# Optimization experiments

Hardware: AMD Instinct MI355X
Metric: run time of the kernel (lower is better)

The kernel has to match this reference:

```python
import jax, jax.numpy as jnp
import numpy as np

B, CIN, COUT, H, W, LAT, G = 4, 128, 256, 64, 64, 256, 16
EPS = 1e-5


def _bn(x, p):
    # p: [4, C] stacked (gamma, beta, running_mean, running_var); eval-mode BN over channel dim 1
    g, b, m, v = p
    sh = (1, -1) + (1,) * (x.ndim - 2)
    return (x - m.reshape(sh)) * (g.reshape(sh) * jax.lax.rsqrt(v.reshape(sh) + EPS)) + b.reshape(sh)


def _prelu(x, a):
    return jnp.where(x > 0, x, a * x)


def _pool(x):
    b, c, h, w = x.shape
    return x.reshape(b, c, h // 2, 2, w // 2, 2).mean((3, 5))


def _conv1x1(w, x):
    return jnp.einsum('oc,bchw->bohw', w, x)


def _cbn(x, latent, bnp, lin):
    y = _bn(x, bnp)
    sb = latent @ lin.T  # [B, 2C]
    s, b = jnp.split(sb, 2, axis=-1)
    return y * s[:, :, None, None] + b[:, :, None, None]


def _axial(x, wqkv, bn_qkv, bn_sim, bn_out, rel, dim):
    # x: [B, C, H, W]; attend along H (dim==0) or W (dim==1)
    x = x.transpose(0, 3, 1, 2) if dim == 0 else x.transpose(0, 2, 1, 3)
    b, d1, c, s = x.shape
    x = x.reshape(b * d1, c, s)
    qkv = _bn(jnp.einsum('oc,bcs->bos', wqkv, x), bn_qkv)  # [bN, 2*COUT, S]
    gc = COUT // G
    qkv = qkv.reshape(b * d1, G, 2 * gc, s)
    q, k, v = qkv[:, :, :gc // 2], qkv[:, :, gc // 2:gc], qkv[:, :, gc:]
    idx = jnp.arange(s)[:, None] - jnp.arange(s)[None, :] + s - 1
    emb = rel[:, idx]  # [2*gc, S, S]
    qe, ke, ve = emb[:gc // 2], emb[gc // 2:gc], emb[gc:]
    q_emb = jnp.einsum('bgci,cij->bgij', q, qe)
    k_emb = jnp.einsum('bgci,cij->bgij', k, ke)
    # torch reinterprets [b,g,S,S] as 'bgci': contraction over the 3rd axis
    qk = jnp.einsum('bgki,bgkj->bgij', q_emb, k_emb)
    sim = jnp.concatenate([qk, q_emb, k_emb], axis=1)  # [bN, 3G, S, S]
    sim = _bn(sim, bn_sim)
    sim = sim.reshape(b * d1, 3, G, s, s).sum(1)
    sim = jax.nn.softmax(sim, axis=-1)
    att = jnp.einsum('bgij,bgcj->bgci', sim, v)
    att_e = jnp.einsum('bgij,cij->bgci', sim, ve)
    o = jnp.stack([att, att_e], axis=3).reshape(b * d1, 2 * COUT, s)
    o = _bn(o, bn_out)
    o = o.reshape(b, d1, COUT, 2, s).sum(3)
    return o.transpose(0, 2, 3, 1) if dim == 0 else o.transpose(0, 2, 1, 3)


def _bn_params(key, c):
    k1, k2, k3, k4 = jax.random.split(key, 4)
    return jnp.stack([1.0 + 0.1 * jax.random.normal(k1, (c,)),
                      0.1 * jax.random.normal(k2, (c,)),
                      0.05 * jax.random.normal(k3, (c,)),
                      jax.random.uniform(k4, (c,), minval=0.5, maxval=1.5)])


def setup_inputs() -> dict:
    key = jax.random.key(0)
    ks = list(jax.random.split(key, 24))
    gc = COUT // G
    inp = {
        'x': jax.random.normal(ks[0], (B, CIN, H, W), dtype=jnp.float32),
        'latent': jax.random.normal(ks[1], (B, LAT), dtype=jnp.float32),
        'w_in': 0.1 * jax.random.normal(ks[2], (COUT, CIN)),
        'bn_in': _bn_params(ks[3], COUT),
        'lin_in': 0.1 * jax.random.normal(ks[4], (2 * COUT, LAT)),
        'alpha_in': jnp.array(0.25, dtype=jnp.float32),
        'a0_wqkv': 0.1 * jax.random.normal(ks[5], (2 * COUT, COUT)),
        'a0_bn_qkv': _bn_params(ks[6], 2 * COUT),
        'a0_bn_sim': _bn_params(ks[7], 3 * G),
        'a0_bn_out': _bn_params(ks[8], 2 * COUT),
        'a0_rel': 0.1 * jax.random.normal(ks[9], (2 * gc, 2 * H - 1)),
        'a1_wqkv': 0.1 * jax.random.normal(ks[10], (2 * COUT, COUT)),
        'a1_bn_qkv': _bn_params(ks[11], 2 * COUT),
        'a1_bn_sim': _bn_params(ks[12], 3 * G),
        'a1_bn_out': _bn_params(ks[13], 2 * COUT),
        'a1_rel': 0.1 * jax.random.normal(ks[14], (2 * gc, 2 * W - 1)),
        'w_out': 0.1 * jax.random.normal(ks[15], (COUT, COUT)),
        'bn_out': _bn_params(ks[16], COUT),
        'lin_out': 0.1 * jax.random.normal(ks[17], (2 * COUT, LAT)),
        'w_res': 0.1 * jax.random.normal(ks[18], (COUT, CIN)),
        'alpha_fin': jnp.array(0.25, dtype=jnp.float32),
    }
    return inp


def reference(x, latent, w_in, bn_in, lin_in, alpha_in,
              a0_wqkv, a0_bn_qkv, a0_bn_sim, a0_bn_out, a0_rel,
              a1_wqkv, a1_bn_qkv, a1_bn_sim, a1_bn_out, a1_rel,
              w_out, bn_out, lin_out, w_res, alpha_fin):
    out = _prelu(_cbn(_conv1x1(w_in, x), latent, bn_in, lin_in), alpha_in)
    out = _axial(out, a0_wqkv, a0_bn_qkv, a0_bn_sim, a0_bn_out, a0_rel, 0)
    out = _axial(out, a1_wqkv, a1_bn_qkv, a1_bn_sim, a1_bn_out, a1_rel, 1)
    out = _cbn(_conv1x1(w_out, _pool(out)), latent, bn_out, lin_out)
    out = out + _pool(_conv1x1(w_res, x))
    return _prelu(out, alpha_fin)
```

## Files before the change

### kernel.cpp

```cpp
#include <hip/hip_runtime.h>
#include <hip/hip_bf16.h>

#define EPS_F 1e-5f

typedef __attribute__((ext_vector_type(8))) _Float16 f16x8;
typedef __attribute__((ext_vector_type(4))) _Float16 f16x4;
typedef __attribute__((ext_vector_type(4))) float f32x4;

union U16x8 { ushort u[8]; _Float16 h[8]; f16x8 v; };

static __device__ inline ushort f2h(float f) {
  _Float16 h = (_Float16)f;
  return __builtin_bit_cast(ushort, h);
}
static __device__ inline float h2f(ushort u) {
  return (float)__builtin_bit_cast(_Float16, u);
}

__global__ void __launch_bounds__(256) prep_kernel(
    const float* __restrict__ w_in, const float* __restrict__ a0w,
    const float* __restrict__ a1w, const float* __restrict__ w_out,
    const float* __restrict__ w_res,
    const float* __restrict__ latent, const float* __restrict__ lin_in,
    const float* __restrict__ lin_out,
    const float* __restrict__ a0_rel, const float* __restrict__ a1_rel,
    const float* __restrict__ x,
    ushort* __restrict__ w16, ushort* __restrict__ relimg,
    float* __restrict__ sb_in, float* __restrict__ sb_out,
    ushort* __restrict__ x16, ushort* __restrict__ pool_x) {
  const int gid = blockIdx.x;
  const int tid = threadIdx.x;
  __shared__ __align__(16) char lsm[10240];

  if (gid < 1608) {
    int idx = gid * 256 + tid;
    if (idx < 393216) {
      const float* src; int off;
      if (idx < 32768)       { src = w_in;  off = 0; }
      else if (idx < 163840) { src = a0w;   off = 32768; }
      else if (idx < 294912) { src = a1w;   off = 163840; }
      else if (idx < 360448) { src = w_out; off = 294912; }
      else                   { src = w_res; off = 360448; }
      w16[idx] = f2h(src[idx - off]);
    } else if (idx < 397312) {
      int r = idx - 393216;
      int which = r >> 11;
      int rr = r & 2047;
      int b = rr >> 9, k = rr & 511;
      const float* lin = which ? lin_out : lin_in;
      const float* lv = latent + b * 256;
      const float* lr = lin + k * 256;
      float acc = 0.f;
#pragma unroll 8
      for (int l = 0; l < 256; ++l) acc += lv[l] * lr[l];
      (which ? sb_out : sb_in)[b * 512 + k] = acc;
    } else if (idx < 411648) {
      int e = idx - 397312;
      int which = e >= 7168;
      int s = which ? e - 7168 : e;
      const float* rel = which ? a1_rel : a0_rel;
      ushort val = 0;
      if (s < 2560) {
        int d = s / 20, c = s % 20;
        if (c < 8 && d < 127) val = f2h(rel[c * 127 + d]);
      } else if (s < 5120) {
        int s2 = s - 2560;
        int d = s2 / 20, c = s2 % 20;
        if (c >= 8 && c < 16 && d < 127) val = f2h(rel[c * 127 + d]);
      } else {
        int pos = (s - 5120) * 2;
        int c = pos >> 8;
        int inner = (pos & 255) ^ ((c & 7) << 4);
        int d = inner >> 1;
        if (d < 127) val = f2h(rel[(16 + c) * 127 + d]);
      }
      relimg[which * 7168 + s] = val;
    }
  } else if (gid < 2120) {
    int e = gid - 1608;
    int pt = e & 31, ct = (e >> 5) & 3, b = e >> 7;
    ushort (*Lt)[40] = (ushort(*)[40])lsm;
#pragma unroll
    for (int r = 0; r < 16; ++r) {
      int e2 = tid + 256 * r;
      int c = e2 >> 7, p = e2 & 127;
      Lt[p][c] = f2h(x[((size_t)(b * 128 + ct * 32 + c)) * 4096 + pt * 128 + p]);
    }
    __syncthreads();
#pragma unroll
    for (int r = 0; r < 2; ++r) {
      int e2 = tid + 256 * r;
      int p = e2 >> 2, q = e2 & 3;
      *(f16x8*)&x16[((size_t)b * 4096 + pt * 128 + p) * 128 + ct * 32 + 8 * q] =
          *(const f16x8*)&Lt[p][8 * q];
    }
  } else {
    int e = gid - 2120;
    int ip = e & 31, ct = (e >> 5) & 3, b = e >> 7;
    float (*Lp)[33] = (float(*)[33])lsm;
    {
      int c = tid >> 3, grp = tid & 7;
      const float* base = x + ((size_t)(b * 128 + ct * 32 + c)) * 4096 + (2 * ip) * 64 + 8 * grp;
      float4 a0 = *(const float4*)&base[0];
      float4 a1 = *(const float4*)&base[4];
      float4 b0 = *(const float4*)&base[64];
      float4 b1 = *(const float4*)&base[68];
      Lp[c][4 * grp + 0] = 0.25f * (a0.x + a0.y + b0.x + b0.y);
      Lp[c][4 * grp + 1] = 0.25f * (a0.z + a0.w + b0.z + b0.w);
      Lp[c][4 * grp + 2] = 0.25f * (a1.x + a1.y + b1.x + b1.y);
      Lp[c][4 * grp + 3] = 0.25f * (a1.z + a1.w + b1.z + b1.w);
    }
    __syncthreads();
    {
      int jp = tid >> 3, q = tid & 7;
      ushort4 o;
      o.x = f2h(Lp[4 * q + 0][jp]);
      o.y = f2h(Lp[4 * q + 1][jp]);
      o.z = f2h(Lp[4 * q + 2][jp]);
      o.w = f2h(Lp[4 * q + 3][jp]);
      *(ushort4*)&pool_x[((size_t)b * 1024 + ip * 32 + jp) * 128 + ct * 32 + 4 * q] = o;
    }
  }
}

template <int MODE>
__global__ void __launch_bounds__(256) conv_mfma_kernel(
    const ushort* __restrict__ X, const ushort* __restrict__ W16,
    ushort* __restrict__ Y16, int Cin, int Cout, int P,
    const float* __restrict__ bn, const float* __restrict__ sb,
    const float* __restrict__ alpha) {
  const int tid = threadIdx.x;
  const int p0 = blockIdx.x * 128;
  const int o0 = blockIdx.y * 64;
  const int b  = blockIdx.z;
  const int lane = tid & 63;
  const int wv = tid >> 6;
  const int m = lane & 15, h = lane >> 4;
  const int wr = wv >> 1, wc = wv & 1;

  __shared__ __align__(16) char smem[27648];
  ushort (*Xs)[72] = (ushort(*)[72])smem;
  ushort (*Ws)[72] = (ushort(*)[72])(smem + 18432);
  ushort (*Es)[72] = (ushort(*)[72])smem;

  f32x4 acc[2][4];
#pragma unroll
  for (int i = 0; i < 2; ++i)
#pragma unroll
    for (int j = 0; j < 4; ++j) acc[i][j] = (f32x4){0.f, 0.f, 0.f, 0.f};

  const ushort* Xb = X + (size_t)b * P * Cin;

  for (int k0 = 0; k0 < Cin; k0 += 64) {
    __syncthreads();
#pragma unroll
    for (int r = 0; r < 4; ++r) {
      int e = tid + 256 * r;
      int pp = e >> 3, ch = e & 7;
      *(f16x8*)&Xs[pp][8 * ch] =
          *(const f16x8*)&Xb[(size_t)(p0 + pp) * Cin + k0 + 8 * ch];
    }
#pragma unroll
    for (int r = 0; r < 2; ++r) {
      int e = tid + 256 * r;
      int oc = e >> 3, ch = e & 7;
      *(f16x8*)&Ws[oc][8 * ch] =
          *(const f16x8*)&W16[(size_t)(o0 + oc) * Cin + k0 + 8 * ch];
    }
    __syncthreads();
#pragma unroll
    for (int ks = 0; ks < 2; ++ks) {
      f16x8 af[2], bf[4];
#pragma unroll
      for (int t = 0; t < 2; ++t) af[t] = *(const f16x8*)&Ws[32 * wr + 16 * t + m][32 * ks + 8 * h];
#pragma unroll
      for (int t = 0; t < 4; ++t) bf[t] = *(const f16x8*)&Xs[64 * wc + 16 * t + m][32 * ks + 8 * h];
#pragma unroll
      for (int ta = 0; ta < 2; ++ta)
#pragma unroll
        for (int tb = 0; tb < 4; ++tb)
          acc[ta][tb] = __builtin_amdgcn_mfma_f32_16x16x32_f16(af[ta], bf[tb], acc[ta][tb], 0, 0, 0);
    }
  }

  float scl[2][4], shf[2][4];
#pragma unroll
  for (int ta = 0; ta < 2; ++ta)
#pragma unroll
    for (int r = 0; r < 4; ++r) {
      int oc = o0 + 32 * wr + 16 * ta + 4 * h + r;
      float scale = 1.f, shift = 0.f;
      if (MODE & 1) {
        float sc = bn[oc] * rsqrtf(bn[3 * Cout + oc] + EPS_F);
        scale = sc;
        shift = bn[Cout + oc] - bn[2 * Cout + oc] * sc;
      }
      if (MODE & 2) {
        float ss = sb[b * 2 * Cout + oc];
        float bb = sb[b * 2 * Cout + Cout + oc];
        scale *= ss;
        shift = shift * ss + bb;
      }
      scl[ta][r] = scale; shf[ta][r] = shift;
    }
  float al = (MODE & 8) ? *alpha : 0.f;

  __syncthreads();
#pragma unroll
  for (int ta = 0; ta < 2; ++ta)
#pragma unroll
    for (int tb = 0; tb < 4; ++tb)
#pragma unroll
      for (int r = 0; r < 4; ++r) {
        float v = acc[ta][tb][r] * scl[ta][r] + shf[ta][r];
        if (MODE & 8) v = v > 0.f ? v : al * v;
        Es[64 * wc + 16 * tb + m][32 * wr + 16 * ta + 4 * h + r] = f2h(v);
      }
  __syncthreads();
#pragma unroll
  for (int r = 0; r < 4; ++r) {
    int e = tid + 256 * r;
    int pp = e >> 3, q = e & 7;
    *(f16x8*)&Y16[((size_t)b * P + p0 + pp) * Cout + o0 + 8 * q] =
        *(const f16x8*)&Es[pp][8 * q];
  }
}

__global__ void __launch_bounds__(256) final_fused_kernel(
    const ushort* __restrict__ t0, const ushort* __restrict__ pool_x,
    const ushort* __restrict__ Wo, const ushort* __restrict__ Wr,
    float* __restrict__ Y32,
    const float* __restrict__ bn, const float* __restrict__ sb,
    const float* __restrict__ alpha) {
  const int tid = threadIdx.x;
  const int p0 = blockIdx.x * 128;
  const int o0 = blockIdx.y * 64;
  const int b  = blockIdx.z;
  const int lane = tid & 63;
  const int wv = tid >> 6;
  const int m = lane & 15, h = lane >> 4;
  const int wr = wv >> 1, wc = wv & 1;

  __shared__ __align__(16) char smem[27648];
  ushort (*Xs)[72] = (ushort(*)[72])smem;
  ushort (*Ws)[72] = (ushort(*)[72])(smem + 18432);

  f32x4 acc1[2][4], acc2[2][4];
#pragma unroll
  for (int i = 0; i < 2; ++i)
#pragma unroll
    for (int j = 0; j < 4; ++j) {
      acc1[i][j] = (f32x4){0.f, 0.f, 0.f, 0.f};
      acc2[i][j] = (f32x4){0.f, 0.f, 0.f, 0.f};
    }

  for (int k0 = 0; k0 < 256; k0 += 64) {
    __syncthreads();
#pragma unroll
    for (int r = 0; r < 4; ++r) {
      int e = tid + 256 * r;
      int pp = e >> 3, ch = e & 7;
      int pg = p0 + pp;
      int ip = pg >> 5, jp = pg & 31;
      size_t tb = ((size_t)b * 4096 + ip * 128 + jp * 2) * 256 + k0 + 8 * ch;
      U16x8 a, bb, c, d, o;
      a.v  = *(const f16x8*)&t0[tb];
      bb.v = *(const f16x8*)&t0[tb + 256];
      c.v  = *(const f16x8*)&t0[tb + 64 * 256];
      d.v  = *(const f16x8*)&t0[tb + 65 * 256];
#pragma unroll
      for (int e2 = 0; e2 < 8; ++e2)
        o.h[e2] = ((a.h[e2] + bb.h[e2]) + (c.h[e2] + d.h[e2])) * (_Float16)0.25f;
      *(f16x8*)&Xs[pp][8 * ch] = o.v;
    }
#pragma unroll
    for (int r = 0; r < 2; ++r) {
      int e = tid + 256 * r;
      int oc = e >> 3, ch = e & 7;
      *(f16x8*)&Ws[oc][8 * ch] = *(const f16x8*)&Wo[(size_t)(o0 + oc) * 256 + k0 + 8 * ch];
    }
    __syncthreads();
#pragma unroll
    for (int ks = 0; ks < 2; ++ks) {
      f16x8 af[2], bf[4];
#pragma unroll
      for (int t = 0; t < 2; ++t) af[t] = *(const f16x8*)&Ws[32 * wr + 16 * t + m][32 * ks + 8 * h];
#pragma unroll
      for (int t = 0; t < 4; ++t) bf[t] = *(const f16x8*)&Xs[64 * wc + 16 * t + m][32 * ks + 8 * h];
#pragma unroll
      for (int ta = 0; ta < 2; ++ta)
#pragma unroll
        for (int tb2 = 0; tb2 < 4; ++tb2)
          acc1[ta][tb2] = __builtin_amdgcn_mfma_f32_16x16x32_f16(af[ta], bf[tb2], acc1[ta][tb2], 0, 0, 0);
    }
  }

  for (int k0 = 0; k0 < 128; k0 += 64) {
    __syncthreads();
#pragma unroll
    for (int r = 0; r < 4; ++r) {
      int e = tid + 256 * r;
      int pp = e >> 3, ch = e & 7;
      *(f16x8*)&Xs[pp][8 * ch] =
          *(const f16x8*)&pool_x[((size_t)b * 1024 + p0 + pp) * 128 + k0 + 8 * ch];
    }
#pragma unroll
    for (int r = 0; r < 2; ++r) {
      int e = tid + 256 * r;
      int oc = e >> 3, ch = e & 7;
      *(f16x8*)&Ws[oc][8 * ch] = *(const f16x8*)&Wr[(size_t)(o0 + oc) * 128 + k0 + 8 * ch];
    }
    __syncthreads();
#pragma unroll
    for (int ks = 0; ks < 2; ++ks) {
      f16x8 af[2], bf[4];
#pragma unroll
      for (int t = 0; t < 2; ++t) af[t] = *(const f16x8*)&Ws[32 * wr + 16 * t + m][32 * ks + 8 * h];
#pragma unroll
      for (int t = 0; t < 4; ++t) bf[t] = *(const f16x8*)&Xs[64 * wc + 16 * t + m][32 * ks + 8 * h];
#pragma unroll
      for (int ta = 0; ta < 2; ++ta)
#pragma unroll
        for (int tb2 = 0; tb2 < 4; ++tb2)
          acc2[ta][tb2] = __builtin_amdgcn_mfma_f32_16x16x32_f16(af[ta], bf[tb2], acc2[ta][tb2], 0, 0, 0);
    }
  }

  const float al = *alpha;
#pragma unroll
  for (int ta = 0; ta < 2; ++ta)
#pragma unroll
    for (int r = 0; r < 4; ++r) {
      int oc = o0 + 32 * wr + 16 * ta + 4 * h + r;
      float sc = bn[oc] * rsqrtf(bn[768 + oc] + EPS_F);
      float shift = bn[256 + oc] - bn[512 + oc] * sc;
      float ss = sb[b * 512 + oc];
      float bb = sb[b * 512 + 256 + oc];
      float scale = sc * ss;
      shift = shift * ss + bb;
#pragma unroll
      for (int tb2 = 0; tb2 < 4; ++tb2) {
        int p = p0 + 64 * wc + 16 * tb2 + m;
        float v = acc1[ta][tb2][r] * scale + shift + acc2[ta][tb2][r];
        v = v > 0.f ? v : al * v;
        Y32[((size_t)b * 256 + oc) * 1024 + p] = v;
      }
    }
}

__global__ void __launch_bounds__(256) axial_attn_kernel(
    const ushort* __restrict__ qkv, const ushort* __restrict__ relimg,
    const float* __restrict__ bn_sim, const float* __restrict__ bn_out,
    ushort* __restrict__ out16) {
  const int tid = threadIdx.x;
  int lin = blockIdx.x;
  int wg = ((lin & 7) << 9) + (lin >> 3);
  const int g  = wg >> 8;
  const int bd = wg & 255;
  const int b  = bd >> 6;
  const int d1 = bd & 63;

  __shared__ __align__(16) char smem[37888];
#define RQA(d, c)  (smem + (d) * 40 + (c) * 2)
#define RKA(d, c)  (smem + 5120 + (d) * 40 + (c) * 2)
#define QKA(i, c)  (smem + 10240 + (i) * 48 + (c) * 2)
#define QEA(i, k)  (smem + 13312 + (i) * 144 + (k) * 2)
#define KEA(j, k)  (smem + 22528 + (j) * 144 + (k) * 2)
#define VCA(c, j)  (smem + 31744 + ((((c) * 128 + (j) * 2)) ^ (((c) & 7) << 4)))
#define RVA(c, d)  (smem + 33792 + ((((c) * 256 + (d) * 2)) ^ (((c) & 7) << 4)))
#define A2A(i, d)  (smem + (i) * 272 + (d) * 2)

  const int lane = tid & 63;
  const int wv   = tid >> 6;
  const int m    = lane & 15;
  const int h    = lane >> 4;

  const int i_ld = tid >> 2, quad = tid & 3;
  f16x8 vld = *(const f16x8*)&qkv[((size_t)b * 4096 + i_ld * 64 + d1) * 512 + g * 32 + 8 * quad];
  {
    const uint4* img = (const uint4*)relimg;
    for (int u = tid; u < 640; u += 256) ((uint4*)smem)[u] = img[u];
    ((uint4*)(smem + 33792))[tid] = img[640 + tid];
  }
  if (quad < 2) {
    *(f16x8*)QKA(i_ld, 8 * quad) = vld;
  } else {
    U16x8 u; u.v = vld;
    int c0 = 8 * (quad - 2);
#pragma unroll
    for (int e = 0; e < 8; ++e) *(ushort*)VCA(c0 + e, i_ld) = u.u[e];
  }
  __syncthreads();

  {
    const int nt = wv;
    const int n = 16 * nt + m;
    f16x4 bqk = *(const f16x4*)QKA(n, 4 * h);
#pragma unroll
    for (int k = 0; k < 5; ++k) {
      int dt = nt + k;
      f16x4 arQ = *(const f16x4*)RQA(16 * dt + m, 4 * h);
      f16x4 arK = *(const f16x4*)RKA(16 * dt + m, 4 * h);
      f32x4 dq = __builtin_amdgcn_mfma_f32_16x16x16f16(arQ, bqk, (f32x4){0.f,0.f,0.f,0.f}, 0, 0, 0);
      f32x4 dk = __builtin_amdgcn_mfma_f32_16x16x16f16(arK, bqk, (f32x4){0.f,0.f,0.f,0.f}, 0, 0, 0);
#pragma unroll
      for (int r = 0; r < 4; ++r) {
        int d = 16 * dt + 4 * h + r;
        int i = n - d + 63;
        if (k == 0 || k == 4) {
          if ((unsigned)i < 64u) {
            *(ushort*)QEA(i, n) = f2h(dq[r]);
            *(ushort*)KEA(i, n) = f2h(dk[r]);
          }
        } else {
          *(ushort*)QEA(i, n) = f2h(dq[r]);
          *(ushort*)KEA(i, n) = f2h(dk[r]);
        }
      }
    }
  }
  __syncthreads();

  f32x4 acc[4];
#pragma unroll
  for (int tj = 0; tj < 4; ++tj) acc[tj] = (f32x4){0.f, 0.f, 0.f, 0.f};
  {
    const int ia = 16 * wv + m;
    f16x8 af0 = *(const f16x8*)QEA(ia, 8 * h);
    f16x8 af1 = *(const f16x8*)QEA(ia, 32 + 8 * h);
#pragma unroll
    for (int tj = 0; tj < 4; ++tj) {
      int j = 16 * tj + m;
      f16x8 bf0 = *(const f16x8*)KEA(j, 8 * h);
      f16x8 bf1 = *(const f16x8*)KEA(j, 32 + 8 * h);
      acc[tj] = __builtin_amdgcn_mfma_f32_16x16x32_f16(af0, bf0, acc[tj], 0, 0, 0);
      acc[tj] = __builtin_amdgcn_mfma_f32_16x16x32_f16(af1, bf1, acc[tj], 0, 0, 0);
    }
  }

  float s_qk = bn_sim[g]      * rsqrtf(bn_sim[144 + g] + EPS_F);
  float s_qe = bn_sim[16 + g] * rsqrtf(bn_sim[160 + g] + EPS_F);
  float s_ke = bn_sim[32 + g] * rsqrtf(bn_sim[176 + g] + EPS_F);
  float sh   = (bn_sim[48 + g] - bn_sim[96 + g]  * s_qk)
             + (bn_sim[64 + g] - bn_sim[112 + g] * s_qe)
             + (bn_sim[80 + g] - bn_sim[128 + g] * s_ke);

  const int ib = 16 * wv + 4 * h;
  float sv[4][4];
#pragma unroll
  for (int tj = 0; tj < 4; ++tj) {
    int j = 16 * tj + m;
    f16x4 qe4 = *(const f16x4*)QEA(j, ib);
    f16x4 ke4 = *(const f16x4*)KEA(j, ib);
#pragma unroll
    for (int r = 0; r < 4; ++r)
      sv[tj][r] = acc[tj][r] * s_qk + (float)qe4[r] * s_qe + (float)ke4[r] * s_ke + sh;
  }

  float p[4][4];
  {
    float mx[4];
#pragma unroll
    for (int r = 0; r < 4; ++r) {
      float v = fmaxf(fmaxf(sv[0][r], sv[1][r]), fmaxf(sv[2][r], sv[3][r]));
      v = fmaxf(v, __shfl_xor(v, 1));
      v = fmaxf(v, __shfl_xor(v, 2));
      v = fmaxf(v, __shfl_xor(v, 4));
      v = fmaxf(v, __shfl_xor(v, 8));
      mx[r] = v;
    }
#pragma unroll
    for (int r = 0; r < 4; ++r) {
      float ssum = 0.f;
#pragma unroll
      for (int tj = 0; tj < 4; ++tj) {
        p[tj][r] = __expf(sv[tj][r] - mx[r]);
        ssum += p[tj][r];
      }
      ssum += __shfl_xor(ssum, 1);
      ssum += __shfl_xor(ssum, 2);
      ssum += __shfl_xor(ssum, 4);
      ssum += __shfl_xor(ssum, 8);
      float inv = 1.f / ssum;
#pragma unroll
      for (int tj = 0; tj < 4; ++tj) p[tj][r] *= inv;
    }
  }

  __syncthreads();

  {
    uint4 z = make_uint4(0u, 0u, 0u, 0u);
    uint4* base = (uint4*)(smem + wv * 4352);
#pragma unroll
    for (int u = 0; u < 4; ++u) base[lane + 64 * u] = z;
    if (lane < 16) base[lane + 256] = z;
  }
#pragma unroll
  for (int tj = 0; tj < 4; ++tj) {
    int j = 16 * tj + m;
#pragma unroll
    for (int r = 0; r < 4; ++r) {
      int i = ib + r;
      *(ushort*)A2A(i, i - j + 63) = f2h(p[tj][r]);
    }
  }

  f32x4 accA = (f32x4){0.f, 0.f, 0.f, 0.f};
  f32x4 accE = (f32x4){0.f, 0.f, 0.f, 0.f};
  {
    const int ia = 16 * wv + m;
#pragma unroll
    for (int ks = 0; ks < 2; ++ks) {
      U16x8 pa;
#pragma unroll
      for (int e = 0; e < 8; ++e) {
        int j = 32 * ks + 8 * h + e;
        pa.u[e] = *(ushort*)A2A(ia, ia - j + 63);
      }
      f16x8 vb = *(const f16x8*)VCA(m, 32 * ks + 8 * h);
      accA = __builtin_amdgcn_mfma_f32_16x16x32_f16(pa.v, vb, accA, 0, 0, 0);
    }
#pragma unroll
    for (int ks = 0; ks < 4; ++ks) {
      f16x8 pe = *(const f16x8*)A2A(ia, 32 * ks + 8 * h);
      f16x8 rv = *(const f16x8*)RVA(m, 32 * ks + 8 * h);
      accE = __builtin_amdgcn_mfma_f32_16x16x32_f16(pe, rv, accE, 0, 0, 0);
    }
  }

  {
    int oc = g * 16 + m;
    int c0 = 2 * oc, c1 = c0 + 1;
    float sc0 = bn_out[c0] * rsqrtf(bn_out[1536 + c0] + EPS_F);
    float sh0 = bn_out[512 + c0] - bn_out[1024 + c0] * sc0;
    float sc1 = bn_out[c1] * rsqrtf(bn_out[1536 + c1] + EPS_F);
    float sh1 = bn_out[512 + c1] - bn_out[1024 + c1] * sc1;
    float vv[4];
    vv[0] = accA[0] * sc0 + accE[0] * sc1 + sh0 + sh1;
    vv[1] = accA[1] * sc0 + accE[1] * sc1 + sh0 + sh1;
    vv[2] = accA[2] * sc0 + accE[2] * sc1 + sh0 + sh1;
    vv[3] = accA[3] * sc0 + accE[3] * sc1 + sh0 + sh1;
    size_t base = ((size_t)b * 4096 + (size_t)d1 * 64 + ib) * 256 + oc;
#pragma unroll
    for (int r = 0; r < 4; ++r)
      out16[base + (size_t)r * 256] = f2h(vv[r]);
  }
#undef RQA
#undef RKA
#undef QKA
#undef QEA
#undef KEA
#undef VCA
#undef RVA
#undef A2A
}

extern "C" void kernel_launch(void* const* d_in, const int* in_sizes, int n_in,
                              void* d_out, int out_size, void* d_ws, size_t ws_size,
                              hipStream_t stream) {
  const float* x         = (const float*)d_in[0];
  const float* latent    = (const float*)d_in[1];
  const float* w_in      = (const float*)d_in[2];
  const float* bn_in     = (const float*)d_in[3];
  const float* lin_in    = (const float*)d_in[4];
  const float* alpha_in  = (const float*)d_in[5];
  const float* a0_wqkv   = (const float*)d_in[6];
  const float* a0_bn_qkv = (const float*)d_in[7];
  const float* a0_bn_sim = (const float*)d_in[8];
  const float* a0_bn_out = (const float*)d_in[9];
  const float* a0_rel    = (const float*)d_in[10];
  const float* a1_wqkv   = (const float*)d_in[11];
  const float* a1_bn_qkv = (const float*)d_in[12];
  const float* a1_bn_sim = (const float*)d_in[13];
  const float* a1_bn_out = (const float*)d_in[14];
  const float* a1_rel    = (const float*)d_in[15];
  const float* w_out     = (const float*)d_in[16];
  const float* bn_outp   = (const float*)d_in[17];
  const float* lin_out   = (const float*)d_in[18];
  const float* w_res     = (const float*)d_in[19];
  const float* alpha_fin = (const float*)d_in[20];

  float* ws = (float*)d_ws;
  float* sb_in  = ws;
  float* sb_out = ws + 2048;
  ushort* w16   = (ushort*)(ws + 4096);
  ushort* relimg = w16 + 393216;
  ushort* x16   = relimg + 14336;
  ushort* t0    = x16 + 2097152;
  ushort* qkvb  = t0 + 4194304;
  ushort* pool_x = qkvb + 8388608;

  ushort* w_in16  = w16;
  ushort* a0w16   = w16 + 32768;
  ushort* a1w16   = w16 + 163840;
  ushort* w_out16 = w16 + 294912;
  ushort* w_res16 = w16 + 360448;
  ushort* rimg_a  = relimg;
  ushort* rimg_b  = relimg + 7168;

  prep_kernel<<<2632, 256, 0, stream>>>(w_in, a0_wqkv, a1_wqkv, w_out, w_res,
                                        latent, lin_in, lin_out, a0_rel, a1_rel,
                                        x, w16, relimg, sb_in, sb_out, x16, pool_x);

  conv_mfma_kernel<11><<<dim3(32, 4, 4), 256, 0, stream>>>(
      x16, w_in16, t0, 128, 256, 4096, bn_in, sb_in, alpha_in);

  conv_mfma_kernel<1><<<dim3(32, 8, 4), 256, 0, stream>>>(
      t0, a0w16, qkvb, 256, 512, 4096, a0_bn_qkv, nullptr, nullptr);
  axial_attn_kernel<<<4096, 256, 0, stream>>>(
      qkvb, rimg_a, a0_bn_sim, a0_bn_out, t0);

  conv_mfma_kernel<1><<<dim3(32, 8, 4), 256, 0, stream>>>(
      t0, a1w16, qkvb, 256, 512, 4096, a1_bn_qkv, nullptr, nullptr);
  axial_attn_kernel<<<4096, 256, 0, stream>>>(
      qkvb, rimg_b, a1_bn_sim, a1_bn_out, t0);

  final_fused_kernel<<<dim3(8, 4, 4), 256, 0, stream>>>(
      t0, pool_x, w_out16, w_res16, (float*)d_out, bn_outp, sb_out, alpha_fin);
}
```

Measured before the change: 140.8 us.

## Fuse QKV projection conv into axial attention kernel

```diff
diff --git a/kernel.cpp b/kernel.cpp
--- a/kernel.cpp
+++ b/kernel.cpp
@@ -8,6 +8,7 @@
 typedef __attribute__((ext_vector_type(4))) float f32x4;
 
 union U16x8 { ushort u[8]; _Float16 h[8]; f16x8 v; };
+union U16x4 { ushort u[4]; f16x4 v; };
 
 static __device__ inline ushort f2h(float f) {
   _Float16 h = (_Float16)f;
@@ -349,14 +350,16 @@
 }
 
 __global__ void __launch_bounds__(256) axial_attn_kernel(
-    const ushort* __restrict__ qkv, const ushort* __restrict__ relimg,
+    const ushort* __restrict__ t0in, const ushort* __restrict__ wqkv,
+    const float* __restrict__ bn_qkv,
+    const ushort* __restrict__ relimg,
     const float* __restrict__ bn_sim, const float* __restrict__ bn_out,
     ushort* __restrict__ out16) {
   const int tid = threadIdx.x;
   int lin = blockIdx.x;
   int wg = ((lin & 7) << 9) + (lin >> 3);
-  const int g  = wg >> 8;
-  const int bd = wg & 255;
+  const int g  = wg & 15;
+  const int bd = wg >> 4;
   const int b  = bd >> 6;
   const int d1 = bd & 63;
 
@@ -364,6 +367,7 @@
 #define RQA(d, c)  (smem + (d) * 40 + (c) * 2)
 #define RKA(d, c)  (smem + 5120 + (d) * 40 + (c) * 2)
 #define QKA(i, c)  (smem + 10240 + (i) * 48 + (c) * 2)
+#define XSA(i, k)  (smem + 13312 + (i) * 144 + (k) * 2)
 #define QEA(i, k)  (smem + 13312 + (i) * 144 + (k) * 2)
 #define KEA(j, k)  (smem + 22528 + (j) * 144 + (k) * 2)
 #define VCA(c, j)  (smem + 31744 + ((((c) * 128 + (j) * 2)) ^ (((c) & 7) << 4)))
@@ -374,21 +378,67 @@
   const int wv   = tid >> 6;
   const int m    = lane & 15;
   const int h    = lane >> 4;
-
-  const int i_ld = tid >> 2, quad = tid & 3;
-  f16x8 vld = *(const f16x8*)&qkv[((size_t)b * 4096 + i_ld * 64 + d1) * 512 + g * 32 + 8 * quad];
+  const int wr   = wv >> 1, wc = wv & 1;
+
   {
     const uint4* img = (const uint4*)relimg;
     for (int u = tid; u < 640; u += 256) ((uint4*)smem)[u] = img[u];
     ((uint4*)(smem + 33792))[tid] = img[640 + tid];
   }
-  if (quad < 2) {
-    *(f16x8*)QKA(i_ld, 8 * quad) = vld;
-  } else {
-    U16x8 u; u.v = vld;
-    int c0 = 8 * (quad - 2);
-#pragma unroll
-    for (int e = 0; e < 8; ++e) *(ushort*)VCA(c0 + e, i_ld) = u.u[e];
+
+  f32x4 cacc[2];
+  cacc[0] = (f32x4){0.f, 0.f, 0.f, 0.f};
+  cacc[1] = (f32x4){0.f, 0.f, 0.f, 0.f};
+  {
+    const ushort* Xb = t0in + ((size_t)b * 4096 + d1) * 256;
+    const ushort* Wg = wqkv + ((size_t)(g * 32 + 16 * wr + m)) * 256;
+    for (int k0 = 0; k0 < 256; k0 += 64) {
+      __syncthreads();
+#pragma unroll
+      for (int r = 0; r < 2; ++r) {
+        int e = tid + 256 * r;
+        int i = e >> 3, sub = e & 7;
+        *(f16x8*)XSA(i, 8 * sub) = *(const f16x8*)&Xb[(size_t)i * 16384 + k0 + 8 * sub];
+      }
+      __syncthreads();
+#pragma unroll
+      for (int ks = 0; ks < 2; ++ks) {
+        f16x8 af = *(const f16x8*)&Wg[k0 + 32 * ks + 8 * h];
+#pragma unroll
+        for (int tb = 0; tb < 2; ++tb) {
+          f16x8 bf = *(const f16x8*)XSA(32 * wc + 16 * tb + m, 32 * ks + 8 * h);
+          cacc[tb] = __builtin_amdgcn_mfma_f32_16x16x32_f16(af, bf, cacc[tb], 0, 0, 0);
+        }
+      }
+    }
+  }
+  {
+    float scl[4], shf[4];
+#pragma unroll
+    for (int r = 0; r < 4; ++r) {
+      int ch = g * 32 + 16 * wr + 4 * h + r;
+      float sc = bn_qkv[ch] * rsqrtf(bn_qkv[1536 + ch] + EPS_F);
+      scl[r] = sc;
+      shf[r] = bn_qkv[512 + ch] - bn_qkv[1024 + ch] * sc;
+    }
+    if (wr == 0) {
+#pragma unroll
+      for (int tb = 0; tb < 2; ++tb) {
+        int i = 32 * wc + 16 * tb + m;
+        U16x4 o;
+#pragma unroll
+        for (int r = 0; r < 4; ++r) o.u[r] = f2h(cacc[tb][r] * scl[r] + shf[r]);
+        *(f16x4*)QKA(i, 4 * h) = o.v;
+      }
+    } else {
+#pragma unroll
+      for (int tb = 0; tb < 2; ++tb) {
+        int i = 32 * wc + 16 * tb + m;
+#pragma unroll
+        for (int r = 0; r < 4; ++r)
+          *(ushort*)VCA(4 * h + r, i) = f2h(cacc[tb][r] * scl[r] + shf[r]);
+      }
+    }
   }
   __syncthreads();
 
@@ -549,6 +599,7 @@
 #undef RQA
 #undef RKA
 #undef QKA
+#undef XSA
 #undef QEA
 #undef KEA
 #undef VCA
@@ -588,8 +639,8 @@
   ushort* relimg = w16 + 393216;
   ushort* x16   = relimg + 14336;
   ushort* t0    = x16 + 2097152;
-  ushort* qkvb  = t0 + 4194304;
-  ushort* pool_x = qkvb + 8388608;
+  ushort* t1    = t0 + 4194304;
+  ushort* pool_x = t1 + 4194304;
 
   ushort* w_in16  = w16;
   ushort* a0w16   = w16 + 32768;
@@ -606,15 +657,11 @@
   conv_mfma_kernel<11><<<dim3(32, 4, 4), 256, 0, stream>>>(
       x16, w_in16, t0, 128, 256, 4096, bn_in, sb_in, alpha_in);
 
-  conv_mfma_kernel<1><<<dim3(32, 8, 4), 256, 0, stream>>>(
-      t0, a0w16, qkvb, 256, 512, 4096, a0_bn_qkv, nullptr, nullptr);
   axial_attn_kernel<<<4096, 256, 0, stream>>>(
-      qkvb, rimg_a, a0_bn_sim, a0_bn_out, t0);
-
-  conv_mfma_kernel<1><<<dim3(32, 8, 4), 256, 0, stream>>>(
-      t0, a1w16, qkvb, 256, 512, 4096, a1_bn_qkv, nullptr, nullptr);
+      t0, a0w16, a0_bn_qkv, rimg_a, a0_bn_sim, a0_bn_out, t1);
+
   axial_attn_kernel<<<4096, 256, 0, stream>>>(
-      qkvb, rimg_b, a1_bn_sim, a1_bn_out, t0);
+      t1, a1w16, a1_bn_qkv, rimg_b, a1_bn_sim, a1_bn_out, t0);
 
   final_fused_kernel<<<dim3(8, 4, 4), 256, 0, stream>>>(
       t0, pool_x, w_out16, w_res16, (float*)d_out, bn_outp, sb_out, alpha_fin);
```

Result: faster. 133.3 us (-5.3%).
